# Performance work log

Measured on AMD Instinct MI355X. Metric: run time of the kernel, lower is better.

Reference implementation:

```python
import jax, jax.numpy as jnp
import numpy as np

TEMPERATURE = 0.07

def l2norm(x, eps=1e-12):
    # torch.nn.functional.normalize(dim=1): x / max(||x||, eps)
    n = jnp.sqrt(jnp.sum(x * x, axis=1, keepdims=True))
    return x / jnp.maximum(n, eps)

def setup_inputs() -> dict:
    key = jax.random.key(0)
    ks = jax.random.split(key, 8)
    B, D_in, H, M, Q, NNEG = 1024, 2048, 1024, 256, 65536, 16384
    return {
        "y1": jax.random.normal(ks[0], (B, D_in), dtype=jnp.float32),
        "y2": jax.random.normal(ks[1], (B, D_in), dtype=jnp.float32),
        "W_enc_q": jax.random.normal(ks[2], (D_in, H), dtype=jnp.float32) * 0.02,
        "W_enc_k": jax.random.normal(ks[3], (D_in, H), dtype=jnp.float32) * 0.02,
        "W_proj": jax.random.normal(ks[4], (H, M), dtype=jnp.float32) * 0.02,
        "queue": jax.random.normal(ks[5], (Q, M), dtype=jnp.float32),
        "sample_idx": jax.random.randint(ks[6], (NNEG,), 0, Q, dtype=jnp.int32),
        "write_idx": jnp.arange(B, dtype=jnp.int32),
    }

def reference(y1, y2, W_enc_q, W_enc_k, W_proj, queue, sample_idx, write_idx):
    # query path (trainable)
    q = l2norm((y2 @ W_enc_q) @ W_proj)                 # [B, M]
    # key path (no_grad in original)
    k = jax.lax.stop_gradient(l2norm((y1 @ W_enc_k) @ W_proj))  # [B, M]
    # sample negatives from GPU-resident queue (gather) + normalize
    neg = l2norm(queue[sample_idx])                     # [NNEG, M]
    pos_logits = jnp.sum(q * k, axis=1, keepdims=True)  # [B, 1]
    neg_logits = q @ neg.T                              # [B, NNEG]
    logits = jnp.concatenate([pos_logits, neg_logits], axis=1) / TEMPERATURE
    # cross_entropy with labels == 0
    loss = -jnp.mean(jax.nn.log_softmax(logits, axis=-1)[:, 0])
    # FIFO append modeled as circular-buffer scatter write
    new_queue = queue.at[write_idx].set(k)
    return loss, new_queue
```

## Files before the change

kernel.cpp:

```cpp
#include <hip/hip_runtime.h>
#include <hip/hip_bf16.h>
#include <math.h>
#include <stdint.h>


typedef __attribute__((ext_vector_type(4))) float floatx4;
typedef __attribute__((ext_vector_type(8))) short bf16x8;
typedef __attribute__((ext_vector_type(8))) unsigned short ushort8;

__device__ __forceinline__ unsigned short f2bf(float x) {
    union { float f; unsigned int u; } v; v.f = x;
    unsigned int r = v.u + 0x7FFFu + ((v.u >> 16) & 1u);
    return (unsigned short)(r >> 16);
}

__device__ __forceinline__ void async_cp16(const void* g, void* l) {
    auto gp = reinterpret_cast<const __attribute__((address_space(1))) unsigned int*>(
        reinterpret_cast<uintptr_t>(g));
    auto lp = reinterpret_cast<__attribute__((address_space(3))) unsigned int*>(
        reinterpret_cast<uintptr_t>(l));
    __builtin_amdgcn_global_load_lds(gp, lp, 16, 0, 0);
}

__global__ __launch_bounds__(256) void prep_small(
    const float* __restrict__ y2, const float* __restrict__ y1,
    unsigned short* __restrict__ y2b, unsigned short* __restrict__ y1b,
    const float* __restrict__ Wq, const float* __restrict__ Wk,
    const float* __restrict__ Wp,
    unsigned short* __restrict__ Wqt, unsigned short* __restrict__ Wkt,
    unsigned short* __restrict__ Wpt,
    int D, int H, int M) {
    __shared__ unsigned short tile[32][33];
    const int b = blockIdx.x, t = threadIdx.x;
    const int nCastY = 1024;
    const int nTW = (D / 32) * (H / 32);

    if (b < 2 * nCastY) {
        const float* in = (b < nCastY) ? y2 : y1;
        unsigned short* outp = (b < nCastY) ? y2b : y1b;
        long i = (long)(b % nCastY) * 256 + t;
        const float4* in4 = (const float4*)in;
        float4 a = in4[i * 2], c = in4[i * 2 + 1];
        ushort8 o;
        o[0] = f2bf(a.x); o[1] = f2bf(a.y); o[2] = f2bf(a.z); o[3] = f2bf(a.w);
        o[4] = f2bf(c.x); o[5] = f2bf(c.y); o[6] = f2bf(c.z); o[7] = f2bf(c.w);
        ((ushort8*)outp)[i] = o;
        return;
    }
    int bb = b - 2 * nCastY;
    const float* in; unsigned short* outp; int R, C, idx;
    if (bb < nTW)           { in = Wq; outp = Wqt; R = D; C = H; idx = bb; }
    else if (bb < 2 * nTW)  { in = Wk; outp = Wkt; R = D; C = H; idx = bb - nTW; }
    else                    { in = Wp; outp = Wpt; R = H; C = M; idx = bb - 2 * nTW; }
    int cb = C / 32;
    int c0 = (idx % cb) * 32, r0 = (idx / cb) * 32;
    int tx = t & 31, ty = t >> 5;
#pragma unroll
    for (int i = 0; i < 4; ++i)
        tile[ty + i * 8][tx] = f2bf(in[(size_t)(r0 + ty + i * 8) * C + c0 + tx]);
    __syncthreads();
#pragma unroll
    for (int i = 0; i < 4; ++i)
        outp[(size_t)(c0 + ty + i * 8) * R + r0 + tx] = tile[tx][ty + i * 8];
}

__global__ __launch_bounds__(256) void enc_plus(
    const unsigned short* __restrict__ Yb,
    const unsigned short* __restrict__ Wt,
    unsigned short* __restrict__ T12b,
    const float4* __restrict__ queue4, float4* __restrict__ newq4,
    const float* __restrict__ queue, const int* __restrict__ sidx,
    unsigned short* __restrict__ negb) {
    __shared__ unsigned short As[2][128 * 32];
    __shared__ unsigned short Bs[2][64 * 32];
    const int b = blockIdx.x, t = threadIdx.x;
    const int type = b % 5, id = b / 5;

    if (type == 0) {
        const int batch = id >> 7, rem = id & 127;
        const int col0 = (rem & 15) * 64, row0 = (rem >> 4) * 128;
        const unsigned short* A = Yb + (long)batch * 1024 * 2048;
        const unsigned short* Bp = Wt + (long)batch * 1024 * 2048;
        unsigned short* C = T12b + (long)batch * 1024 * 1024;
        const int Ko = 2048, No = 1024;
        const int lane = t & 63, wave = t >> 6;
        const int wr = wave >> 1, wc = wave & 1;
        const int lrow = lane & 15, quad = lane >> 4;
        const int nK = Ko / 32;

        floatx4 acc[4][2] = {};

        auto stage = [&](int kk, int p) {
            int c0 = t, c1 = t + 256;
            async_cp16(A + (size_t)(row0 + (c0 >> 2)) * Ko + kk + (c0 & 3) * 8,
                       (char*)(As[p]) + (size_t)c0 * 16);
            async_cp16(A + (size_t)(row0 + (c1 >> 2)) * Ko + kk + (c1 & 3) * 8,
                       (char*)(As[p]) + (size_t)c1 * 16);
            async_cp16(Bp + (size_t)(col0 + (t >> 2)) * Ko + kk + (t & 3) * 8,
                       (char*)(Bs[p]) + (size_t)t * 16);
        };
        auto compute = [&](int p) {
            bf16x8 af[4], bfr[2];
#pragma unroll
            for (int i = 0; i < 4; ++i)
                af[i] = *(const bf16x8*)(As[p] + (size_t)(wr * 64 + i * 16 + lrow) * 32 + quad * 8);
#pragma unroll
            for (int j = 0; j < 2; ++j)
                bfr[j] = *(const bf16x8*)(Bs[p] + (size_t)(wc * 32 + j * 16 + lrow) * 32 + quad * 8);
            __builtin_amdgcn_s_setprio(1);
#pragma unroll
            for (int i = 0; i < 4; ++i)
#pragma unroll
                for (int j = 0; j < 2; ++j)
                    acc[i][j] = __builtin_amdgcn_mfma_f32_16x16x32_bf16(af[i], bfr[j], acc[i][j], 0, 0, 0);
            __builtin_amdgcn_s_setprio(0);
        };

        stage(0, 0);
#pragma unroll 2
        for (int k = 0; k < nK - 1; ++k) {
            stage((k + 1) * 32, (k & 1) ^ 1);
            asm volatile("s_waitcnt vmcnt(3)" ::: "memory");
            __builtin_amdgcn_s_barrier();
            compute(k & 1);
            __builtin_amdgcn_s_barrier();
        }
        asm volatile("s_waitcnt vmcnt(0)" ::: "memory");
        __builtin_amdgcn_s_barrier();
        compute((nK - 1) & 1);

#pragma unroll
        for (int i = 0; i < 4; ++i) {
            int grow = row0 + wr * 64 + i * 16 + quad * 4;
#pragma unroll
            for (int j = 0; j < 2; ++j) {
                int gcol = col0 + wc * 32 + j * 16 + lrow;
#pragma unroll
                for (int r = 0; r < 4; ++r)
                    C[(size_t)(grow + r) * No + gcol] = f2bf(acc[i][j][r]);
            }
        }
    } else if (type == 2 || type == 4) {
        const int gid = id * 2 + (type == 4);
        const int w = t >> 6, lane = t & 63;
#pragma unroll
        for (int j = 0; j < 8; ++j) {
            int r = gid * 32 + w * 8 + j;
            const float4* src = (const float4*)(queue + (size_t)sidx[r] * 256);
            float4 v = src[lane];
            float ss = v.x * v.x + v.y * v.y + v.z * v.z + v.w * v.w;
#pragma unroll
            for (int off = 1; off < 64; off <<= 1) ss += __shfl_xor(ss, off);
            float inv = 1.f / fmaxf(sqrtf(ss), 1e-12f);
            unsigned short o[4] = { f2bf(v.x * inv), f2bf(v.y * inv),
                                    f2bf(v.z * inv), f2bf(v.w * inv) };
            *(unsigned long long*)(negb + (size_t)r * 256 + lane * 4) =
                *(unsigned long long*)o;
        }
    } else {
        const int cid = id * 2 + (type == 3);
        long base = (long)cid * 8192 + t;
#pragma unroll
        for (int o = 0; o < 4; ++o) {
            float4 v[8];
#pragma unroll
            for (int i = 0; i < 8; ++i) v[i] = queue4[base + (size_t)(o * 8 + i) * 256];
#pragma unroll
            for (int i = 0; i < 8; ++i) newq4[base + (size_t)(o * 8 + i) * 256] = v[i];
        }
    }
}

__global__ __launch_bounds__(256) void gemm_proj(const unsigned short* __restrict__ Ag,
                                                 const unsigned short* __restrict__ Bg,
                                                 float* __restrict__ Pg,
                                                 int No, int Ko, int nsplit,
                                                 long sAb) {
    __shared__ unsigned short As[2][128 * 32];
    __shared__ unsigned short Bs[2][64 * 32];
    const int z = blockIdx.z;
    const int batch = z / nsplit, split = z - batch * nsplit;
    const unsigned short* A = Ag + (long)batch * sAb;
    const unsigned short* B = Bg;
    float* P = Pg + (long)z * 1024 * No;
    const int Kc = Ko / nsplit, kbeg = split * Kc;
    const int row0 = blockIdx.y * 128, col0 = blockIdx.x * 64;
    const int t = threadIdx.x;
    const int lane = t & 63, wave = t >> 6;
    const int wr = wave >> 1, wc = wave & 1;
    const int lrow = lane & 15, quad = lane >> 4;
    const int nIt = Kc / 32;

    floatx4 acc[4][2] = {};

    auto stage = [&](int kk, int p) {
        int c0 = t, c1 = t + 256;
        async_cp16(A + (size_t)(row0 + (c0 >> 2)) * Ko + kk + (c0 & 3) * 8,
                   (char*)(As[p]) + (size_t)c0 * 16);
        async_cp16(A + (size_t)(row0 + (c1 >> 2)) * Ko + kk + (c1 & 3) * 8,
                   (char*)(As[p]) + (size_t)c1 * 16);
        async_cp16(B + (size_t)(col0 + (t >> 2)) * Ko + kk + (t & 3) * 8,
                   (char*)(Bs[p]) + (size_t)t * 16);
    };
    auto compute = [&](int p) {
        bf16x8 af[4], bfr[2];
#pragma unroll
        for (int i = 0; i < 4; ++i)
            af[i] = *(const bf16x8*)(As[p] + (size_t)(wr * 64 + i * 16 + lrow) * 32 + quad * 8);
#pragma unroll
        for (int j = 0; j < 2; ++j)
            bfr[j] = *(const bf16x8*)(Bs[p] + (size_t)(wc * 32 + j * 16 + lrow) * 32 + quad * 8);
        __builtin_amdgcn_s_setprio(1);
#pragma unroll
        for (int i = 0; i < 4; ++i)
#pragma unroll
            for (int j = 0; j < 2; ++j)
                acc[i][j] = __builtin_amdgcn_mfma_f32_16x16x32_bf16(af[i], bfr[j], acc[i][j], 0, 0, 0);
        __builtin_amdgcn_s_setprio(0);
    };

    stage(kbeg, 0);
    for (int k = 0; k < nIt - 1; ++k) {
        stage(kbeg + (k + 1) * 32, (k & 1) ^ 1);
        asm volatile("s_waitcnt vmcnt(3)" ::: "memory");
        __builtin_amdgcn_s_barrier();
        compute(k & 1);
        __builtin_amdgcn_s_barrier();
    }
    asm volatile("s_waitcnt vmcnt(0)" ::: "memory");
    __builtin_amdgcn_s_barrier();
    compute((nIt - 1) & 1);

#pragma unroll
    for (int i = 0; i < 4; ++i) {
        int grow = row0 + wr * 64 + i * 16 + quad * 4;
#pragma unroll
        for (int j = 0; j < 2; ++j) {
            int gcol = col0 + wc * 32 + j * 16 + lrow;
#pragma unroll
            for (int r = 0; r < 4; ++r)
                P[(size_t)(grow + r) * No + gcol] = acc[i][j][r];
        }
    }
}

__global__ __launch_bounds__(256) void qk_finalize(const float* __restrict__ P,
                                                   const int* __restrict__ widx,
                                                   unsigned short* __restrict__ qkb,
                                                   float* __restrict__ newq,
                                                   float* __restrict__ pos,
                                                   float* __restrict__ sumexp,
                                                   int B_, int nsplit, float invT) {
    const int i = blockIdx.x, t = threadIdx.x;
    const long RM = (long)B_ * 256;
    float sq = 0.f, sk = 0.f;
    for (int s = 0; s < nsplit; ++s) {
        sq += P[(long)s * RM + (long)i * 256 + t];
        sk += P[(long)(nsplit + s) * RM + (long)i * 256 + t];
    }
    __shared__ float r0[256], r1[256], r2[256];
    r0[t] = sq * sq; r1[t] = sk * sk; r2[t] = sq * sk;
    __syncthreads();
    for (int off = 128; off > 0; off >>= 1) {
        if (t < off) { r0[t] += r0[t + off]; r1[t] += r1[t + off]; r2[t] += r2[t + off]; }
        __syncthreads();
    }
    float nq = fmaxf(sqrtf(r0[0]), 1e-12f);
    float nk = fmaxf(sqrtf(r1[0]), 1e-12f);
    float qn = sq / nq, kn = sk / nk;
    qkb[(size_t)i * 256 + t] = f2bf(qn);
    qkb[(size_t)(B_ + i) * 256 + t] = f2bf(kn);
    newq[(size_t)widx[i] * 256 + t] = kn;
    if (t == 0) {
        float p = (r2[0] / (nq * nk)) * invT;
        pos[i] = p;
        sumexp[i] = __expf(p);
    }
}

__global__ __launch_bounds__(256) void gemm_logits(const unsigned short* __restrict__ A,
                                                   const unsigned short* __restrict__ B,
                                                   float* __restrict__ sumexp,
                                                   int Ko, float invT) {
    __shared__ unsigned short As[128 * 64];
    __shared__ unsigned short Bs[128 * 64];
    __shared__ float rowred[128];
    const int row0 = blockIdx.y * 128, col0 = blockIdx.x * 128;
    const int t = threadIdx.x;
    const int lane = t & 63, wave = t >> 6;
    const int wr = wave >> 1, wc = wave & 1;
    const int lrow = lane & 15, quad = lane >> 4;

    floatx4 acc[4][4] = {};

    for (int kk = 0; kk < Ko; kk += 64) {
#pragma unroll
        for (int r = 0; r < 4; ++r) {
            int c = t + r * 256;
            async_cp16(A + (size_t)(row0 + (c >> 3)) * Ko + kk + (c & 7) * 8,
                       (char*)As + (size_t)c * 16);
            async_cp16(B + (size_t)(col0 + (c >> 3)) * Ko + kk + (c & 7) * 8,
                       (char*)Bs + (size_t)c * 16);
        }
        __syncthreads();
        bf16x8 af[4][2], bf[4][2];
#pragma unroll
        for (int i = 0; i < 4; ++i)
#pragma unroll
            for (int k2 = 0; k2 < 2; ++k2) {
                af[i][k2] = *(const bf16x8*)(As + (size_t)(wr * 64 + i * 16 + lrow) * 64 + k2 * 32 + quad * 8);
                bf[i][k2] = *(const bf16x8*)(Bs + (size_t)(wc * 64 + i * 16 + lrow) * 64 + k2 * 32 + quad * 8);
            }
#pragma unroll
        for (int k2 = 0; k2 < 2; ++k2)
#pragma unroll
            for (int i = 0; i < 4; ++i)
#pragma unroll
                for (int j = 0; j < 4; ++j)
                    acc[i][j] = __builtin_amdgcn_mfma_f32_16x16x32_bf16(af[i][k2], bf[j][k2], acc[i][j], 0, 0, 0);
        __syncthreads();
    }
    if (t < 128) rowred[t] = 0.f;
    __syncthreads();
#pragma unroll
    for (int i = 0; i < 4; ++i) {
#pragma unroll
        for (int r = 0; r < 4; ++r) {
            float s = 0.f;
#pragma unroll
            for (int j = 0; j < 4; ++j) s += __expf(acc[i][j][r] * invT);
            s += __shfl_xor(s, 1); s += __shfl_xor(s, 2);
            s += __shfl_xor(s, 4); s += __shfl_xor(s, 8);
            if (lrow == 0) atomicAdd(&rowred[wr * 64 + i * 16 + quad * 4 + r], s);
        }
    }
    __syncthreads();
    if (t < 128) atomicAdd(&sumexp[row0 + t], rowred[t]);
}

__global__ __launch_bounds__(256) void final_loss(const float* __restrict__ pos,
                                                  const float* __restrict__ sumexp,
                                                  float* __restrict__ out, int B_) {
    const int t = threadIdx.x;
    float acc = 0.f;
    for (int i = t; i < B_; i += 256) acc += logf(sumexp[i]) - pos[i];
    __shared__ float s[256];
    s[t] = acc;
    __syncthreads();
    for (int off = 128; off > 0; off >>= 1) {
        if (t < off) s[t] += s[t + off];
        __syncthreads();
    }
    if (t == 0) out[0] = s[0] / (float)B_;
}

extern "C" void kernel_launch(void* const* d_in, const int* in_sizes, int n_in,
                              void* d_out, int out_size, void* d_ws, size_t ws_size,
                              hipStream_t stream) {
    const float* y1    = (const float*)d_in[0];
    const float* y2    = (const float*)d_in[1];
    const float* Wq    = (const float*)d_in[2];
    const float* Wk    = (const float*)d_in[3];
    const float* Wp    = (const float*)d_in[4];
    const float* queue = (const float*)d_in[5];
    const int*   sidx  = (const int*)d_in[6];
    const int*   widx  = (const int*)d_in[7];
    float* out = (float*)d_out;

    const int B    = in_sizes[7];
    const int NNEG = in_sizes[6];
    const int D    = in_sizes[0] / B;
    const int H    = in_sizes[2] / D;
    const int M    = in_sizes[4] / H;
    const int Q    = in_sizes[5] / M;
    const float invT = 1.0f / 0.07f;
    const int NS_P = 4;

    float* ws  = (float*)d_ws;
    float* Pp     = ws;
    float* pos    = Pp + (size_t)2 * NS_P * B * M;
    float* sumexp = pos + B;
    unsigned short* us = (unsigned short*)(sumexp + B);
    unsigned short* y2b  = us;
    unsigned short* y1b  = y2b + (size_t)B * D;
    unsigned short* Wqt  = y1b + (size_t)B * D;
    unsigned short* Wkt  = Wqt + (size_t)H * D;
    unsigned short* Wpt  = Wkt + (size_t)H * D;
    unsigned short* T12b = Wpt + (size_t)M * H;
    unsigned short* qkb  = T12b + (size_t)2 * B * H;
    unsigned short* negb = qkb + (size_t)2 * B * M;

    const int nPrep = 2 * 1024 + 2 * (D / 32) * (H / 32) + (H / 32) * (M / 32);
    prep_small<<<nPrep, 256, 0, stream>>>(y2, y1, y2b, y1b, Wq, Wk, Wp,
                                          Wqt, Wkt, Wpt, D, H, M);

    enc_plus<<<1280, 256, 0, stream>>>(y2b, Wqt, T12b,
                                       (const float4*)queue, (float4*)(out + 1),
                                       queue, sidx, negb);

    gemm_proj<<<dim3(M / 64, B / 128, 2 * NS_P), 256, 0, stream>>>(
        T12b, Wpt, Pp, M, H, NS_P, (long)B * H);

    qk_finalize<<<B, 256, 0, stream>>>(Pp, widx, qkb, out + 1, pos, sumexp,
                                       B, NS_P, invT);

    gemm_logits<<<dim3(NNEG / 128, B / 128), 256, 0, stream>>>(
        qkb, negb, sumexp, M, invT);

    final_loss<<<1, 256, 0, stream>>>(pos, sumexp, out, B);
}
```

Before: 228.7 us.

## Reassociate encoder chain to precompute combined projection weights before batch GEMM

Computes Wc = (W_enc @ W_proj)^T first (256x2048 per path), then multiplies the inputs by it, replacing the B x D x H encoder GEMM followed by the H x M projection. This removes the large intermediate T12 and most of the FLOPs. The weights are now cast without a transpose, the GEMMs use a three-stage async load pipeline, and the queue copy and negative gather are spread across the new kernels. Rounding the combined weights to bf16 changes numerics slightly.

```diff
diff --git a/kernel.cpp b/kernel.cpp
--- a/kernel.cpp
+++ b/kernel.cpp
@@ -22,71 +22,66 @@
     __builtin_amdgcn_global_load_lds(gp, lp, 16, 0, 0);
 }
 
-__global__ __launch_bounds__(256) void prep_small(
+__global__ __launch_bounds__(256) void prep_all(
     const float* __restrict__ y2, const float* __restrict__ y1,
-    unsigned short* __restrict__ y2b, unsigned short* __restrict__ y1b,
     const float* __restrict__ Wq, const float* __restrict__ Wk,
     const float* __restrict__ Wp,
-    unsigned short* __restrict__ Wqt, unsigned short* __restrict__ Wkt,
+    unsigned short* __restrict__ y2b, unsigned short* __restrict__ y1b,
+    unsigned short* __restrict__ Wqb, unsigned short* __restrict__ Wkb,
     unsigned short* __restrict__ Wpt,
     int D, int H, int M) {
     __shared__ unsigned short tile[32][33];
     const int b = blockIdx.x, t = threadIdx.x;
-    const int nCastY = 1024;
-    const int nTW = (D / 32) * (H / 32);
-
-    if (b < 2 * nCastY) {
-        const float* in = (b < nCastY) ? y2 : y1;
-        unsigned short* outp = (b < nCastY) ? y2b : y1b;
-        long i = (long)(b % nCastY) * 256 + t;
+
+    if (b < 4096) {
+        const int g = b >> 10, i = b & 1023;
+        const float* in = (g == 0) ? y2 : (g == 1) ? y1 : (g == 2) ? Wq : Wk;
+        unsigned short* outp = (g == 0) ? y2b : (g == 1) ? y1b : (g == 2) ? Wqb : Wkb;
+        long idx = (long)i * 256 + t;
         const float4* in4 = (const float4*)in;
-        float4 a = in4[i * 2], c = in4[i * 2 + 1];
+        float4 a = in4[idx * 2], c = in4[idx * 2 + 1];
         ushort8 o;
         o[0] = f2bf(a.x); o[1] = f2bf(a.y); o[2] = f2bf(a.z); o[3] = f2bf(a.w);
         o[4] = f2bf(c.x); o[5] = f2bf(c.y); o[6] = f2bf(c.z); o[7] = f2bf(c.w);
-        ((ushort8*)outp)[i] = o;
+        ((ushort8*)outp)[idx] = o;
         return;
     }
-    int bb = b - 2 * nCastY;
-    const float* in; unsigned short* outp; int R, C, idx;
-    if (bb < nTW)           { in = Wq; outp = Wqt; R = D; C = H; idx = bb; }
-    else if (bb < 2 * nTW)  { in = Wk; outp = Wkt; R = D; C = H; idx = bb - nTW; }
-    else                    { in = Wp; outp = Wpt; R = H; C = M; idx = bb - 2 * nTW; }
+    int idx = b - 4096;
+    const int R = H, C = M;
     int cb = C / 32;
     int c0 = (idx % cb) * 32, r0 = (idx / cb) * 32;
     int tx = t & 31, ty = t >> 5;
 #pragma unroll
     for (int i = 0; i < 4; ++i)
-        tile[ty + i * 8][tx] = f2bf(in[(size_t)(r0 + ty + i * 8) * C + c0 + tx]);
+        tile[ty + i * 8][tx] = f2bf(Wp[(size_t)(r0 + ty + i * 8) * C + c0 + tx]);
     __syncthreads();
 #pragma unroll
     for (int i = 0; i < 4; ++i)
-        outp[(size_t)(c0 + ty + i * 8) * R + r0 + tx] = tile[tx][ty + i * 8];
-}
-
-__global__ __launch_bounds__(256) void enc_plus(
-    const unsigned short* __restrict__ Yb,
-    const unsigned short* __restrict__ Wt,
-    unsigned short* __restrict__ T12b,
-    const float4* __restrict__ queue4, float4* __restrict__ newq4,
+        Wpt[(size_t)(c0 + ty + i * 8) * R + r0 + tx] = tile[tx][ty + i * 8];
+}
+
+__global__ __launch_bounds__(256) void wc_plus(
+    const unsigned short* __restrict__ Wpt,
+    const unsigned short* __restrict__ Wqkb,
+    unsigned short* __restrict__ Wct,
     const float* __restrict__ queue, const int* __restrict__ sidx,
     unsigned short* __restrict__ negb) {
-    __shared__ unsigned short As[2][128 * 32];
-    __shared__ unsigned short Bs[2][64 * 32];
+    __shared__ unsigned short As[3][128 * 32];
+    __shared__ unsigned short Bs[3][64 * 32];
     const int b = blockIdx.x, t = threadIdx.x;
-    const int type = b % 5, id = b / 5;
+    const int type = b % 3, id = b / 3;
 
     if (type == 0) {
-        const int batch = id >> 7, rem = id & 127;
-        const int col0 = (rem & 15) * 64, row0 = (rem >> 4) * 128;
-        const unsigned short* A = Yb + (long)batch * 1024 * 2048;
-        const unsigned short* Bp = Wt + (long)batch * 1024 * 2048;
-        unsigned short* C = T12b + (long)batch * 1024 * 1024;
-        const int Ko = 2048, No = 1024;
+        const int batch = id >> 6, rem = id & 63;
+        const int row0 = (rem >> 5) * 128;
+        const int col0 = (rem & 31) * 64;
+        const unsigned short* A = Wpt;
+        const unsigned short* Bp = Wqkb + (long)batch * 2048 * 1024;
+        unsigned short* C = Wct + (long)batch * 256 * 2048;
+        const int Ko = 1024, No = 2048, nIt = 32;
         const int lane = t & 63, wave = t >> 6;
         const int wr = wave >> 1, wc = wave & 1;
         const int lrow = lane & 15, quad = lane >> 4;
-        const int nK = Ko / 32;
 
         floatx4 acc[4][2] = {};
 
@@ -117,18 +112,20 @@
         };
 
         stage(0, 0);
-#pragma unroll 2
-        for (int k = 0; k < nK - 1; ++k) {
-            stage((k + 1) * 32, (k & 1) ^ 1);
-            asm volatile("s_waitcnt vmcnt(3)" ::: "memory");
+        stage(32, 1);
+        for (int k = 0; k < nIt; ++k) {
+            if (k + 2 < nIt) {
+                stage((k + 2) * 32, (k + 2) % 3);
+                asm volatile("s_waitcnt vmcnt(6)" ::: "memory");
+            } else if (k + 2 == nIt) {
+                asm volatile("s_waitcnt vmcnt(3)" ::: "memory");
+            } else {
+                asm volatile("s_waitcnt vmcnt(0)" ::: "memory");
+            }
             __builtin_amdgcn_s_barrier();
-            compute(k & 1);
+            compute(k % 3);
             __builtin_amdgcn_s_barrier();
         }
-        asm volatile("s_waitcnt vmcnt(0)" ::: "memory");
-        __builtin_amdgcn_s_barrier();
-        compute((nK - 1) & 1);
-
 #pragma unroll
         for (int i = 0; i < 4; ++i) {
             int grow = row0 + wr * 64 + i * 16 + quad * 4;
@@ -140,12 +137,12 @@
                     C[(size_t)(grow + r) * No + gcol] = f2bf(acc[i][j][r]);
             }
         }
-    } else if (type == 2 || type == 4) {
-        const int gid = id * 2 + (type == 4);
+    } else {
+        const int gid = id * 2 + (type == 2);
         const int w = t >> 6, lane = t & 63;
 #pragma unroll
-        for (int j = 0; j < 8; ++j) {
-            int r = gid * 32 + w * 8 + j;
+        for (int j = 0; j < 16; ++j) {
+            int r = gid * 64 + w * 16 + j;
             const float4* src = (const float4*)(queue + (size_t)sidx[r] * 256);
             float4 v = src[lane];
             float ss = v.x * v.x + v.y * v.y + v.z * v.z + v.w * v.w;
@@ -157,8 +154,89 @@
             *(unsigned long long*)(negb + (size_t)r * 256 + lane * 4) =
                 *(unsigned long long*)o;
         }
+    }
+}
+
+__global__ __launch_bounds__(256) void qk_plus(
+    const unsigned short* __restrict__ Yb,
+    const unsigned short* __restrict__ Wct,
+    float* __restrict__ Pg,
+    const float4* __restrict__ queue4, float4* __restrict__ newq4) {
+    __shared__ unsigned short As[3][128 * 32];
+    __shared__ unsigned short Bs[3][64 * 32];
+    const int b = blockIdx.x, t = threadIdx.x;
+    const int type = b % 3, id = b / 3;
+
+    if (type == 0) {
+        const int z = id >> 5, rem = id & 31;
+        const int batch = z >> 2, split = z & 3;
+        const int row0 = (rem >> 2) * 128;
+        const int col0 = (rem & 3) * 64;
+        const unsigned short* A = Yb + (long)batch * 1024 * 2048;
+        const unsigned short* Bp = Wct + (long)batch * 256 * 2048;
+        float* P = Pg + (long)z * 1024 * 256;
+        const int Ko = 2048, No = 256, nIt = 16;
+        const int kbeg = split * 512;
+        const int lane = t & 63, wave = t >> 6;
+        const int wr = wave >> 1, wc = wave & 1;
+        const int lrow = lane & 15, quad = lane >> 4;
+
+        floatx4 acc[4][2] = {};
+
+        auto stage = [&](int kk, int p) {
+            int c0 = t, c1 = t + 256;
+            async_cp16(A + (size_t)(row0 + (c0 >> 2)) * Ko + kk + (c0 & 3) * 8,
+                       (char*)(As[p]) + (size_t)c0 * 16);
+            async_cp16(A + (size_t)(row0 + (c1 >> 2)) * Ko + kk + (c1 & 3) * 8,
+                       (char*)(As[p]) + (size_t)c1 * 16);
+            async_cp16(Bp + (size_t)(col0 + (t >> 2)) * Ko + kk + (t & 3) * 8,
+                       (char*)(Bs[p]) + (size_t)t * 16);
+        };
+        auto compute = [&](int p) {
+            bf16x8 af[4], bfr[2];
+#pragma unroll
+            for (int i = 0; i < 4; ++i)
+                af[i] = *(const bf16x8*)(As[p] + (size_t)(wr * 64 + i * 16 + lrow) * 32 + quad * 8);
+#pragma unroll
+            for (int j = 0; j < 2; ++j)
+                bfr[j] = *(const bf16x8*)(Bs[p] + (size_t)(wc * 32 + j * 16 + lrow) * 32 + quad * 8);
+            __builtin_amdgcn_s_setprio(1);
+#pragma unroll
+            for (int i = 0; i < 4; ++i)
+#pragma unroll
+                for (int j = 0; j < 2; ++j)
+                    acc[i][j] = __builtin_amdgcn_mfma_f32_16x16x32_bf16(af[i], bfr[j], acc[i][j], 0, 0, 0);
+            __builtin_amdgcn_s_setprio(0);
+        };
+
+        stage(kbeg, 0);
+        stage(kbeg + 32, 1);
+        for (int k = 0; k < nIt; ++k) {
+            if (k + 2 < nIt) {
+                stage(kbeg + (k + 2) * 32, (k + 2) % 3);
+                asm volatile("s_waitcnt vmcnt(6)" ::: "memory");
+            } else if (k + 2 == nIt) {
+                asm volatile("s_waitcnt vmcnt(3)" ::: "memory");
+            } else {
+                asm volatile("s_waitcnt vmcnt(0)" ::: "memory");
+            }
+            __builtin_amdgcn_s_barrier();
+            compute(k % 3);
+            __builtin_amdgcn_s_barrier();
+        }
+#pragma unroll
+        for (int i = 0; i < 4; ++i) {
+            int grow = row0 + wr * 64 + i * 16 + quad * 4;
+#pragma unroll
+            for (int j = 0; j < 2; ++j) {
+                int gcol = col0 + wc * 32 + j * 16 + lrow;
+#pragma unroll
+                for (int r = 0; r < 4; ++r)
+                    P[(size_t)(grow + r) * No + gcol] = acc[i][j][r];
+            }
+        }
     } else {
-        const int cid = id * 2 + (type == 3);
+        const int cid = id * 2 + (type == 2);
         long base = (long)cid * 8192 + t;
 #pragma unroll
         for (int o = 0; o < 4; ++o) {
@@ -167,79 +245,6 @@
             for (int i = 0; i < 8; ++i) v[i] = queue4[base + (size_t)(o * 8 + i) * 256];
 #pragma unroll
             for (int i = 0; i < 8; ++i) newq4[base + (size_t)(o * 8 + i) * 256] = v[i];
-        }
-    }
-}
-
-__global__ __launch_bounds__(256) void gemm_proj(const unsigned short* __restrict__ Ag,
-                                                 const unsigned short* __restrict__ Bg,
-                                                 float* __restrict__ Pg,
-                                                 int No, int Ko, int nsplit,
-                                                 long sAb) {
-    __shared__ unsigned short As[2][128 * 32];
-    __shared__ unsigned short Bs[2][64 * 32];
-    const int z = blockIdx.z;
-    const int batch = z / nsplit, split = z - batch * nsplit;
-    const unsigned short* A = Ag + (long)batch * sAb;
-    const unsigned short* B = Bg;
-    float* P = Pg + (long)z * 1024 * No;
-    const int Kc = Ko / nsplit, kbeg = split * Kc;
-    const int row0 = blockIdx.y * 128, col0 = blockIdx.x * 64;
-    const int t = threadIdx.x;
-    const int lane = t & 63, wave = t >> 6;
-    const int wr = wave >> 1, wc = wave & 1;
-    const int lrow = lane & 15, quad = lane >> 4;
-    const int nIt = Kc / 32;
-
-    floatx4 acc[4][2] = {};
-
-    auto stage = [&](int kk, int p) {
-        int c0 = t, c1 = t + 256;
-        async_cp16(A + (size_t)(row0 + (c0 >> 2)) * Ko + kk + (c0 & 3) * 8,
-                   (char*)(As[p]) + (size_t)c0 * 16);
-        async_cp16(A + (size_t)(row0 + (c1 >> 2)) * Ko + kk + (c1 & 3) * 8,
-                   (char*)(As[p]) + (size_t)c1 * 16);
-        async_cp16(B + (size_t)(col0 + (t >> 2)) * Ko + kk + (t & 3) * 8,
-                   (char*)(Bs[p]) + (size_t)t * 16);
-    };
-    auto compute = [&](int p) {
-        bf16x8 af[4], bfr[2];
-#pragma unroll
-        for (int i = 0; i < 4; ++i)
-            af[i] = *(const bf16x8*)(As[p] + (size_t)(wr * 64 + i * 16 + lrow) * 32 + quad * 8);
-#pragma unroll
-        for (int j = 0; j < 2; ++j)
-            bfr[j] = *(const bf16x8*)(Bs[p] + (size_t)(wc * 32 + j * 16 + lrow) * 32 + quad * 8);
-        __builtin_amdgcn_s_setprio(1);
-#pragma unroll
-        for (int i = 0; i < 4; ++i)
-#pragma unroll
-            for (int j = 0; j < 2; ++j)
-                acc[i][j] = __builtin_amdgcn_mfma_f32_16x16x32_bf16(af[i], bfr[j], acc[i][j], 0, 0, 0);
-        __builtin_amdgcn_s_setprio(0);
-    };
-
-    stage(kbeg, 0);
-    for (int k = 0; k < nIt - 1; ++k) {
-        stage(kbeg + (k + 1) * 32, (k & 1) ^ 1);
-        asm volatile("s_waitcnt vmcnt(3)" ::: "memory");
-        __builtin_amdgcn_s_barrier();
-        compute(k & 1);
-        __builtin_amdgcn_s_barrier();
-    }
-    asm volatile("s_waitcnt vmcnt(0)" ::: "memory");
-    __builtin_amdgcn_s_barrier();
-    compute((nIt - 1) & 1);
-
-#pragma unroll
-    for (int i = 0; i < 4; ++i) {
-        int grow = row0 + wr * 64 + i * 16 + quad * 4;
-#pragma unroll
-        for (int j = 0; j < 2; ++j) {
-            int gcol = col0 + wc * 32 + j * 16 + lrow;
-#pragma unroll
-            for (int r = 0; r < 4; ++r)
-                P[(size_t)(grow + r) * No + gcol] = acc[i][j][r];
         }
     }
 }
@@ -372,7 +377,6 @@
     const int D    = in_sizes[0] / B;
     const int H    = in_sizes[2] / D;
     const int M    = in_sizes[4] / H;
-    const int Q    = in_sizes[5] / M;
     const float invT = 1.0f / 0.07f;
     const int NS_P = 4;
 
@@ -383,23 +387,21 @@
     unsigned short* us = (unsigned short*)(sumexp + B);
     unsigned short* y2b  = us;
     unsigned short* y1b  = y2b + (size_t)B * D;
-    unsigned short* Wqt  = y1b + (size_t)B * D;
-    unsigned short* Wkt  = Wqt + (size_t)H * D;
-    unsigned short* Wpt  = Wkt + (size_t)H * D;
-    unsigned short* T12b = Wpt + (size_t)M * H;
-    unsigned short* qkb  = T12b + (size_t)2 * B * H;
+    unsigned short* Wqb  = y1b + (size_t)B * D;
+    unsigned short* Wkb  = Wqb + (size_t)D * H;
+    unsigned short* Wpt  = Wkb + (size_t)D * H;
+    unsigned short* Wct  = Wpt + (size_t)M * H;
+    unsigned short* qkb  = Wct + (size_t)2 * M * D;
     unsigned short* negb = qkb + (size_t)2 * B * M;
 
-    const int nPrep = 2 * 1024 + 2 * (D / 32) * (H / 32) + (H / 32) * (M / 32);
-    prep_small<<<nPrep, 256, 0, stream>>>(y2, y1, y2b, y1b, Wq, Wk, Wp,
-                                          Wqt, Wkt, Wpt, D, H, M);
-
-    enc_plus<<<1280, 256, 0, stream>>>(y2b, Wqt, T12b,
-                                       (const float4*)queue, (float4*)(out + 1),
-                                       queue, sidx, negb);
-
-    gemm_proj<<<dim3(M / 64, B / 128, 2 * NS_P), 256, 0, stream>>>(
-        T12b, Wpt, Pp, M, H, NS_P, (long)B * H);
+    const int nPrep = 4 * 1024 + (H / 32) * (M / 32);
+    prep_all<<<nPrep, 256, 0, stream>>>(y2, y1, Wq, Wk, Wp,
+                                        y2b, y1b, Wqb, Wkb, Wpt, D, H, M);
+
+    wc_plus<<<384, 256, 0, stream>>>(Wpt, Wqb, Wct, queue, sidx, negb);
+
+    qk_plus<<<768, 256, 0, stream>>>(y2b, Wct, Pp,
+                                     (const float4*)queue, (float4*)(out + 1));
 
     qk_finalize<<<B, 256, 0, stream>>>(Pp, widx, qkb, out + 1, pos, sumexp,
                                        B, NS_P, invT);
```

After: 216.6 us. 1.06x faster.
